# Kernel tuning notes

Hardware: AMD Instinct MI355X
Metric: run time of the kernel (lower is better)

The kernel has to match this reference:

```python
import jax, jax.numpy as jnp
import numpy as np

N = 6000; E = 96000; DIN = 3000; FH1 = 256; FH2 = 128; GH = 128; LAT = 256
K = 10; SCALE = 9; NC = 10; AT = 0.5; ALPHA = 1.0; BN_EPS = 1e-4

# eval-mode BatchNorm1d with running_mean=0, running_var=1
def _bn(x, g, b):
    return x * (g / jnp.sqrt(1.0 + BN_EPS)) + b

def _block(x, W, bb, g, be):  # Linear + BN(eval) + ELU (dropout=identity in eval)
    return jax.nn.elu(_bn(x @ W + bb, g, be))

def _tconv(x, src, dst, Wq, Wk, Wv, Ws, bq, bk, bv, bs):
    # PyG TransformerConv, heads=1, root_weight=True, eval (no dropout)
    q = x @ Wq + bq; k = x @ Wk + bk; v = x @ Wv + bv
    sc = 1.0 / jnp.sqrt(jnp.asarray(q.shape[-1], x.dtype))
    logit = jnp.sum(q[dst] * k[src], axis=-1) * sc            # [E]
    m = jax.ops.segment_max(logit, dst, num_segments=N)
    e = jnp.exp(logit - m[dst])
    s = jax.ops.segment_sum(e, dst, num_segments=N)
    alpha = e / s[dst]                                        # softmax over incoming edges
    out = jax.ops.segment_sum(alpha[:, None] * v[src], dst, num_segments=N) + x @ Ws + bs
    return out, alpha

def _dense_adj(src, dst, alpha):
    # remove_self_loops + to_dense_adj: dense[src, dst] += alpha for src != dst
    mask = (src != dst).astype(alpha.dtype)
    return jnp.zeros((N, N), alpha.dtype).at[src, dst].add(alpha * mask)

def _encode(x, adj, adjp, ew1, eb1, eg1, ebe1, ew2, eb2, eg2, ebe2,
            cWq, cWk, cWv, cWs, cbq, cbk, cbv, cbs):
    feat = _block(_block(x, ew1, eb1, eg1, ebe1), ew2, eb2, eg2, ebe2)
    h = feat
    lastAp = None
    for l in range(3):
        o, a = _tconv(h, adj[0], adj[1], cWq[l], cWk[l], cWv[l], cWs[l], cbq[l], cbk[l], cbv[l], cbs[l])
        # middle layer applies the 'prue' conv to the freshly produced x (as in source)
        hp_in = o if l == 1 else h
        op, ap = _tconv(hp_in, adjp[0], adjp[1], cWq[l], cWk[l], cWv[l], cWs[l], cbq[l], cbk[l], cbv[l], cbs[l])
        A = _dense_adj(adj[0], adj[1], a)
        Ap = _dense_adj(adjp[0], adjp[1], ap)
        h = (1.0 - AT) * (A @ o) + AT * (Ap @ op)
        if l < 2:
            h = jax.nn.relu(h)
        lastAp = Ap
    return h, feat, lastAp

def setup_inputs():
    key = jax.random.key(0)
    ks = jax.random.split(key, 24)
    w = lambda k, sh, fan: (jax.random.normal(k, sh, jnp.float32) / np.sqrt(fan)).astype(jnp.float32)
    inp = {}
    inp['x'] = jax.random.normal(ks[0], (N, DIN), jnp.float32)
    inp['x_neighbor'] = jax.random.normal(ks[1], (N, DIN), jnp.float32)
    inp['spatial'] = jax.random.uniform(ks[2], (N, 2), jnp.float32)
    inp['adj'] = jax.random.randint(ks[3], (2, E), 0, N, dtype=jnp.int32)
    inp['adj_prue'] = jax.random.randint(ks[4], (2, E), 0, N, dtype=jnp.int32)
    # encoder
    inp['enc_W1'] = w(ks[5], (DIN, FH1), DIN); inp['enc_b1'] = jnp.zeros((FH1,))
    inp['enc_g1'] = jnp.ones((FH1,)); inp['enc_be1'] = jnp.zeros((FH1,))
    inp['enc_W2'] = w(ks[6], (FH1, FH2), FH1); inp['enc_b2'] = jnp.zeros((FH2,))
    inp['enc_g2'] = jnp.ones((FH2,)); inp['enc_be2'] = jnp.zeros((FH2,))
    # 3 TransformerConv layers (gc1, conv_hidden[0], gc2) all 128->128: stacked
    inp['conv_Wq'] = w(ks[7], (3, GH, GH), GH); inp['conv_Wk'] = w(ks[8], (3, GH, GH), GH)
    inp['conv_Wv'] = w(ks[9], (3, GH, GH), GH); inp['conv_Ws'] = w(ks[10], (3, GH, GH), GH)
    inp['conv_bq'] = jnp.zeros((3, GH)); inp['conv_bk'] = jnp.zeros((3, GH))
    inp['conv_bv'] = jnp.zeros((3, GH)); inp['conv_bs'] = jnp.zeros((3, GH))
    # decoder
    inp['dec_W'] = w(ks[11], (LAT, DIN), LAT); inp['dec_b'] = jnp.zeros((DIN,))
    inp['dec_g'] = jnp.ones((DIN,)); inp['dec_be'] = jnp.zeros((DIN,))
    inp['cluster'] = w(ks[12], (NC, LAT), LAT)
    return inp

def reference(x, x_neighbor, spatial, enc_W1, enc_b1, enc_g1, enc_be1,
              enc_W2, enc_b2, enc_g2, enc_be2,
              conv_Wq, conv_Wk, conv_Wv, conv_Ws, conv_bq, conv_bk, conv_bv, conv_bs,
              dec_W, dec_b, dec_g, dec_be, cluster, adj, adj_prue):
    enc = (enc_W1, enc_b1, enc_g1, enc_be1, enc_W2, enc_b2, enc_g2, enc_be2)
    conv = (conv_Wq, conv_Wk, conv_Wv, conv_Ws, conv_bq, conv_bk, conv_bv, conv_bs)
    mu, feat_x, atten = _encode(x, adj, adj_prue, *enc, *conv)
    mu_nb, feat_nb, _ = _encode(x_neighbor, adj, adj_prue, *enc, *conv)
    z = jnp.concatenate([feat_x, mu], axis=1)          # [N, LAT]
    z_nb = jnp.concatenate([feat_nb, mu_nb], axis=1)
    # Graph_spatial: kNN in joint feature+spatial space (dense [N,N] distances)
    df = (jnp.sum(z * z, 1)[:, None] - 2.0 * (z @ z_nb.T) + jnp.sum(z_nb * z_nb, 1)[None, :])
    ds = (jnp.sum(spatial * spatial, 1)[:, None] - 2.0 * (spatial @ spatial.T)
          + jnp.sum(spatial * spatial, 1)[None, :])
    neg_top, idx_k = jax.lax.top_k(-(df + ds), K)      # [N, K]
    score_k = jax.nn.softmax(neg_top, axis=-1)
    # GCNBlock_spatial: gather scale=9 nearest neighbor features and aggregate
    idx9 = idx_k[:, :SCALE]
    x_h = z_nb[idx9]                                   # [N, 9, LAT]
    wgt = score_k[:, :SCALE]
    wgt = wgt / jnp.sum(wgt, axis=-1, keepdims=True)
    z_out = z + jnp.einsum('nk,nkd->nd', wgt, x_h)     # x1_lr
    x1_hr = (x_h * wgt[:, :, None]).reshape(N * SCALE, LAT)
    de_feat = _block(z_out, dec_W, dec_b, dec_g, dec_be)
    # student-t cluster assignment
    d2 = jnp.sum((z_out[:, None, :] - cluster[None, :, :]) ** 2, axis=2)
    q = (1.0 / (1.0 + d2 / ALPHA)) ** ((ALPHA + 1.0) / 2.0)
    q = q / jnp.sum(q, axis=1, keepdims=True)
    return (z_out, de_feat, q, feat_x, de_feat, x1_hr, atten)
```

## Files before the change

kernel.cpp:

```cpp
#include <hip/hip_runtime.h>
#include <hip/hip_bf16.h>
#include <math.h>
#include <stdint.h>

#define NN 6000
#define NE 96000
#define KDIN 3000
#define NCAND 12
#define NTILE 47
#define TCAND (NCAND*NTILE)
#define PRE 32

#define OFF_ZOUT 0
#define OFF_DE1  1536000
#define OFF_Q    19536000
#define OFF_FEAT 19596000
#define OFF_DE2  20364000
#define OFF_X1   38364000
#define OFF_ATT  52188000

typedef __attribute__((ext_vector_type(8))) short short8;
typedef __attribute__((ext_vector_type(4))) float f32x4;

__device__ __forceinline__ unsigned short f2bf(float f){
  unsigned int u = __float_as_uint(f);
  u += 0x7FFFu + ((u >> 16) & 1u);
  return (unsigned short)(u >> 16);
}
__device__ __forceinline__ float bf2f(unsigned short h){
  return __uint_as_float(((unsigned int)h) << 16);
}

__global__ void prep_k(const float* __restrict__ W1, const float* __restrict__ W2,
                       const float* __restrict__ Wq, const float* __restrict__ Wk,
                       const float* __restrict__ Wv, const float* __restrict__ Ws,
                       const float* __restrict__ bq, const float* __restrict__ bk,
                       const float* __restrict__ bv, const float* __restrict__ bs,
                       const float* __restrict__ decW, const float* __restrict__ spat,
                       double* __restrict__ W1t, double* __restrict__ W2t,
                       double* __restrict__ Bct, float* __restrict__ Dt,
                       double* __restrict__ bcat,
                       double* __restrict__ sx64, double* __restrict__ sy64,
                       double* __restrict__ ssq64,
                       float* __restrict__ sx32, float* __restrict__ sy32)
{
  int t = blockIdx.x * 256 + threadIdx.x;
  if (t < 768000){
    int n = t / 3000, k = t % 3000;
    W1t[t] = (double)W1[(size_t)k * 256 + n]; return;
  }
  t -= 768000;
  if (t < 32768){
    int n = t / 256, k = t % 256;
    W2t[t] = (double)W2[(size_t)k * 128 + n]; return;
  }
  t -= 32768;
  if (t < 196608){
    int l = t / 65536; int rem = t % 65536;
    int n = rem / 128, k = rem % 128;
    int sel = n >> 7, nn = n & 127;
    const float* Wm = sel==0 ? Wq : sel==1 ? Wk : sel==2 ? Wv : Ws;
    Bct[t] = (double)Wm[((size_t)(l*128) + k) * 128 + nn]; return;
  }
  t -= 196608;
  if (t < 768000){
    int n = t / 256, k = t % 256;
    Dt[t] = decW[(size_t)k * 3000 + n]; return;
  }
  t -= 768000;
  if (t < 1536){
    int l = t / 512, n = t % 512;
    int sel = n >> 7, nn = n & 127;
    const float* bm = sel==0 ? bq : sel==1 ? bk : sel==2 ? bv : bs;
    bcat[t] = (double)bm[l*128 + nn]; return;
  }
  t -= 1536;
  if (t < NN){
    float sx = spat[(size_t)t*2], sy = spat[(size_t)t*2+1];
    sx64[t]=(double)sx; sy64[t]=(double)sy;
    ssq64[t]=(double)sx*(double)sx + (double)sy*(double)sy;
    sx32[t]=sx; sy32[t]=sy; return;
  }
}

__global__ void castup_k(const float* __restrict__ s, double* __restrict__ d, int n){
  int t = blockIdx.x*256 + threadIdx.x;
  if (t < n) d[t] = (double)s[t];
}

__global__ void splitz_k(const double* __restrict__ z64, unsigned short* __restrict__ zh,
                         unsigned short* __restrict__ zl, int n){
  int t = blockIdx.x*256 + threadIdx.x;
  if (t < n){
    float v = (float)z64[t];
    unsigned short h = f2bf(v);
    float r = v - bf2f(h);
    zh[t] = h; zl[t] = f2bf(r);
  }
}

template<int EPI, typename TA>
__global__ __launch_bounds__(256)
void gemm64_k(const TA* __restrict__ A, int lda,
              const double* __restrict__ Bt, int ldb,
              int M, int K, int Ncol,
              double* __restrict__ outF, int ldc,
              const double* __restrict__ bias,
              const float* __restrict__ gam, const float* __restrict__ bet,
              double* __restrict__ outF2)
{
  __shared__ double lA[64][18];
  __shared__ double lB[64][18];
  const int tid = threadIdx.x;
  const int m0 = blockIdx.y * 64;
  const int n0 = blockIdx.x * 64;
  const int tx = tid & 15;
  const int ty = tid >> 4;

  double acc[4][4];
  #pragma unroll
  for (int i=0;i<4;i++)
    #pragma unroll
    for (int j=0;j<4;j++) acc[i][j] = 0.0;

  const int nkt = (K + 15) >> 4;
  for (int kt = 0; kt < nkt; kt++){
    const int k0 = kt << 4;
    __syncthreads();
    #pragma unroll
    for (int c=0;c<4;c++){
      int lin = tid + c*256;
      int row = lin >> 4, col = lin & 15;
      int gm = m0 + row, gk = k0 + col;
      double va = 0.0, vb = 0.0;
      if (gm < M && gk < K)        va = (double)A [(size_t)gm*lda + gk];
      if (n0+row < Ncol && gk < K) vb = Bt[(size_t)(n0+row)*ldb + gk];
      lA[row][col] = va;
      lB[row][col] = vb;
    }
    __syncthreads();
    #pragma unroll 4
    for (int kk=0; kk<16; kk+=2){
      double2 A0 = *(const double2*)&lA[ty   ][kk];
      double2 A1 = *(const double2*)&lA[ty+16][kk];
      double2 A2 = *(const double2*)&lA[ty+32][kk];
      double2 A3 = *(const double2*)&lA[ty+48][kk];
      double2 B0 = *(const double2*)&lB[tx   ][kk];
      double2 B1 = *(const double2*)&lB[tx+16][kk];
      double2 B2 = *(const double2*)&lB[tx+32][kk];
      double2 B3 = *(const double2*)&lB[tx+48][kk];
      acc[0][0]+=A0.x*B0.x; acc[0][1]+=A0.x*B1.x; acc[0][2]+=A0.x*B2.x; acc[0][3]+=A0.x*B3.x;
      acc[1][0]+=A1.x*B0.x; acc[1][1]+=A1.x*B1.x; acc[1][2]+=A1.x*B2.x; acc[1][3]+=A1.x*B3.x;
      acc[2][0]+=A2.x*B0.x; acc[2][1]+=A2.x*B1.x; acc[2][2]+=A2.x*B2.x; acc[2][3]+=A2.x*B3.x;
      acc[3][0]+=A3.x*B0.x; acc[3][1]+=A3.x*B1.x; acc[3][2]+=A3.x*B2.x; acc[3][3]+=A3.x*B3.x;
      acc[0][0]+=A0.y*B0.y; acc[0][1]+=A0.y*B1.y; acc[0][2]+=A0.y*B2.y; acc[0][3]+=A0.y*B3.y;
      acc[1][0]+=A1.y*B0.y; acc[1][1]+=A1.y*B1.y; acc[1][2]+=A1.y*B2.y; acc[1][3]+=A1.y*B3.y;
      acc[2][0]+=A2.y*B0.y; acc[2][1]+=A2.y*B1.y; acc[2][2]+=A2.y*B2.y; acc[2][3]+=A2.y*B3.y;
      acc[3][0]+=A3.y*B0.y; acc[3][1]+=A3.y*B1.y; acc[3][2]+=A3.y*B2.y; acc[3][3]+=A3.y*B3.y;
    }
  }
  #pragma unroll
  for (int j=0;j<4;j++){
    int gn = n0 + tx + 16*j;
    if (gn >= Ncol) continue;
    double bi = bias[gn];
    #pragma unroll
    for (int i=0;i<4;i++){
      int gm = m0 + ty + 16*i;
      if (gm >= M) continue;
      double v = acc[i][j] + bi;
      outF[(size_t)gm*ldc + gn] = v;
      if (outF2) outF2[(size_t)gm*ldc + gn] = v;
    }
  }
}

template<typename TA>
__global__ __launch_bounds__(256)
void gemm64s_k(const TA* __restrict__ A, int lda,
               const double* __restrict__ Bt, int ldb,
               int M, int K, int kchunk, int Ncol,
               double* __restrict__ part)
{
  __shared__ double lA[64][18];
  __shared__ double lB[64][18];
  const int tid = threadIdx.x;
  const int m0 = blockIdx.y * 64;
  const int n0 = blockIdx.x * 64;
  const int tx = tid & 15;
  const int ty = tid >> 4;
  const int kbeg = blockIdx.z * kchunk;
  const int kend = min(K, kbeg + kchunk);
  double* dst = part + (size_t)blockIdx.z * M * Ncol;

  double acc[4][4];
  #pragma unroll
  for (int i=0;i<4;i++)
    #pragma unroll
    for (int j=0;j<4;j++) acc[i][j] = 0.0;

  const int nkt = (kend - kbeg + 15) >> 4;
  for (int kt = 0; kt < nkt; kt++){
    const int k0 = kbeg + (kt << 4);
    __syncthreads();
    #pragma unroll
    for (int c=0;c<4;c++){
      int lin = tid + c*256;
      int row = lin >> 4, col = lin & 15;
      int gm = m0 + row, gk = k0 + col;
      double va = 0.0, vb = 0.0;
      if (gm < M && gk < kend)        va = (double)A [(size_t)gm*lda + gk];
      if (n0+row < Ncol && gk < kend) vb = Bt[(size_t)(n0+row)*ldb + gk];
      lA[row][col] = va;
      lB[row][col] = vb;
    }
    __syncthreads();
    #pragma unroll 4
    for (int kk=0; kk<16; kk+=2){
      double2 A0 = *(const double2*)&lA[ty   ][kk];
      double2 A1 = *(const double2*)&lA[ty+16][kk];
      double2 A2 = *(const double2*)&lA[ty+32][kk];
      double2 A3 = *(const double2*)&lA[ty+48][kk];
      double2 B0 = *(const double2*)&lB[tx   ][kk];
      double2 B1 = *(const double2*)&lB[tx+16][kk];
      double2 B2 = *(const double2*)&lB[tx+32][kk];
      double2 B3 = *(const double2*)&lB[tx+48][kk];
      acc[0][0]+=A0.x*B0.x; acc[0][1]+=A0.x*B1.x; acc[0][2]+=A0.x*B2.x; acc[0][3]+=A0.x*B3.x;
      acc[1][0]+=A1.x*B0.x; acc[1][1]+=A1.x*B1.x; acc[1][2]+=A1.x*B2.x; acc[1][3]+=A1.x*B3.x;
      acc[2][0]+=A2.x*B0.x; acc[2][1]+=A2.x*B1.x; acc[2][2]+=A2.x*B2.x; acc[2][3]+=A2.x*B3.x;
      acc[3][0]+=A3.x*B0.x; acc[3][1]+=A3.x*B1.x; acc[3][2]+=A3.x*B2.x; acc[3][3]+=A3.x*B3.x;
      acc[0][0]+=A0.y*B0.y; acc[0][1]+=A0.y*B1.y; acc[0][2]+=A0.y*B2.y; acc[0][3]+=A0.y*B3.y;
      acc[1][0]+=A1.y*B0.y; acc[1][1]+=A1.y*B1.y; acc[1][2]+=A1.y*B2.y; acc[1][3]+=A1.y*B3.y;
      acc[2][0]+=A2.y*B0.y; acc[2][1]+=A2.y*B1.y; acc[2][2]+=A2.y*B2.y; acc[2][3]+=A2.y*B3.y;
      acc[3][0]+=A3.y*B0.y; acc[3][1]+=A3.y*B1.y; acc[3][2]+=A3.y*B2.y; acc[3][3]+=A3.y*B3.y;
    }
  }
  #pragma unroll
  for (int j=0;j<4;j++){
    int gn = n0 + tx + 16*j;
    if (gn >= Ncol) continue;
    #pragma unroll
    for (int i=0;i<4;i++){
      int gm = m0 + ty + 16*i;
      if (gm >= M) continue;
      dst[(size_t)gm*Ncol + gn] = acc[i][j];
    }
  }
}

__global__ void epi64_k(const double* __restrict__ part, int nsplit, size_t pstride,
                        int M, int Ncol, const double* __restrict__ bias,
                        const float* __restrict__ gam, const float* __restrict__ bet,
                        double* __restrict__ out, int ldo)
{
  int t = blockIdx.x*256 + threadIdx.x;
  if (t >= M*Ncol) return;
  int gm = t / Ncol, gn = t - gm*Ncol;
  double v = 0.0;
  for (int s=0; s<nsplit; s++) v += part[(size_t)s*pstride + t];
  const double BNS = 0.99995000374968755261;
  v += bias[gn];
  v = v * ((double)gam[gn]*BNS) + (double)bet[gn];
  v = v > 0.0 ? v : expm1(v);
  out[(size_t)gm*ldo + gn] = v;
}

__global__ __launch_bounds__(256)
void gemm32d_k(const float* __restrict__ A, int lda,
               const float* __restrict__ Bt, int ldb,
               int M, int K, int Ncol,
               float* __restrict__ out1, int ldc,
               const float* __restrict__ bias, const float* __restrict__ gam,
               const float* __restrict__ bet, float* __restrict__ out2)
{
  __shared__ float lA[64][33];
  __shared__ float lB[64][33];
  const int tid = threadIdx.x;
  const int m0 = blockIdx.y * 64;
  const int n0 = blockIdx.x * 64;
  const int tx = tid & 15;
  const int ty = tid >> 4;

  float acc[4][4];
  #pragma unroll
  for (int i=0;i<4;i++)
    #pragma unroll
    for (int j=0;j<4;j++) acc[i][j] = 0.f;

  const int nkt = (K + 31) >> 5;
  for (int kt = 0; kt < nkt; kt++){
    const int k0 = kt << 5;
    __syncthreads();
    #pragma unroll
    for (int c=0;c<8;c++){
      int lin = tid + c*256;
      int row = lin >> 5, col = lin & 31;
      int gm = m0 + row, gk = k0 + col;
      float va = 0.f, vb = 0.f;
      if (gm < M && gk < K)        va = A [(size_t)gm*lda + gk];
      if (n0+row < Ncol && gk < K) vb = Bt[(size_t)(n0+row)*ldb + gk];
      lA[row][col] = va;
      lB[row][col] = vb;
    }
    __syncthreads();
    #pragma unroll 4
    for (int kk=0; kk<32; kk++){
      float a0=lA[ty][kk], a1=lA[ty+16][kk], a2=lA[ty+32][kk], a3=lA[ty+48][kk];
      float b0=lB[tx][kk], b1=lB[tx+16][kk], b2=lB[tx+32][kk], b3=lB[tx+48][kk];
      acc[0][0]+=a0*b0; acc[0][1]+=a0*b1; acc[0][2]+=a0*b2; acc[0][3]+=a0*b3;
      acc[1][0]+=a1*b0; acc[1][1]+=a1*b1; acc[1][2]+=a1*b2; acc[1][3]+=a1*b3;
      acc[2][0]+=a2*b0; acc[2][1]+=a2*b1; acc[2][2]+=a2*b2; acc[2][3]+=a2*b3;
      acc[3][0]+=a3*b0; acc[3][1]+=a3*b1; acc[3][2]+=a3*b2; acc[3][3]+=a3*b3;
    }
  }
  const float BNS = 0.99995000374968755f;
  #pragma unroll
  for (int j=0;j<4;j++){
    int gn = n0 + tx + 16*j;
    if (gn >= Ncol) continue;
    float bi = bias[gn];
    float gs = gam[gn]*BNS, be = bet[gn];
    #pragma unroll
    for (int i=0;i<4;i++){
      int gm = m0 + ty + 16*i;
      if (gm >= M) continue;
      float v = acc[i][j] + bi;
      v = v*gs + be; v = v > 0.f ? v : expm1f(v);
      out1[(size_t)gm*ldc + gn] = v;
      out2[(size_t)gm*ldc + gn] = v;
    }
  }
}

__global__ void csr_cnt_k(const int* __restrict__ key, int* __restrict__ cnt){
  int e = blockIdx.x*256 + threadIdx.x;
  if (e < NE) atomicAdd(&cnt[key[e]], 1);
}
__global__ __launch_bounds__(256)
void csr_scan_k(const int* __restrict__ cnt, int* __restrict__ rowptr, int* __restrict__ cursor){
  __shared__ int part[256];
  int t = threadIdx.x;
  int base = t*24;
  int loc[24]; int s=0;
  #pragma unroll
  for (int u=0;u<24;u++){
    int idx = base+u;
    int v = (idx<NN) ? cnt[idx] : 0;
    loc[u] = s; s += v;
  }
  part[t] = s;
  __syncthreads();
  if (t==0){
    int run=0;
    for (int u=0;u<256;u++){ int tmp=part[u]; part[u]=run; run+=tmp; }
  }
  __syncthreads();
  int off = part[t];
  #pragma unroll
  for (int u=0;u<24;u++){
    int idx = base+u;
    if (idx<NN){ rowptr[idx]=off+loc[u]; cursor[idx]=off+loc[u]; }
  }
  if (t==255) rowptr[NN] = off + s;
}
__global__ void csr_fill_k(const int* __restrict__ key, int* __restrict__ cursor,
                           int* __restrict__ elist){
  int e = blockIdx.x*256 + threadIdx.x;
  if (e < NE){ int pos = atomicAdd(&cursor[key[e]], 1); elist[pos] = e; }
}

__global__ __launch_bounds__(256)
void attn_k(double* __restrict__ QKVS, const int* __restrict__ rowptr,
            const int* __restrict__ elist, const int* __restrict__ src,
            double* __restrict__ alpha)
{
  __shared__ double lg[4][128];
  const int w = threadIdx.x >> 6;
  const int node = blockIdx.x*4 + w;
  if (node >= NN) return;
  const int lane = threadIdx.x & 63;
  const int e0 = rowptr[node], e1 = rowptr[node+1];
  const int deg = e1 - e0;
  if (deg <= 0) return;
  const double SC = 0.088388347648318447;
  const double* q = QKVS + (size_t)node*512;
  double q0 = q[lane], q1 = q[lane+64];

  if (deg <= 128){
    double m = -1.0e300;
    for (int i=0;i<deg;i++){
      const double* k = QKVS + (size_t)src[elist[e0+i]]*512 + 128;
      double p = q0*k[lane] + q1*k[lane+64];
      #pragma unroll
      for (int off=32; off; off>>=1) p += __shfl_xor(p, off);
      p *= SC;
      if (lane==0) lg[w][i] = p;
      m = fmax(m, p);
    }
    double S = 0.0;
    for (int i=0;i<deg;i++){
      double ex = exp(lg[w][i] - m);
      if (lane==0) lg[w][i] = ex;
      S += ex;
    }
    double inv = 1.0 / S;
    double o0 = QKVS[(size_t)node*512 + 384 + lane];
    double o1 = QKVS[(size_t)node*512 + 448 + lane];
    for (int i=0;i<deg;i++){
      int e = elist[e0+i];
      double a = lg[w][i] * inv;
      const double* v = QKVS + (size_t)src[e]*512 + 256;
      o0 = fma(a, v[lane],    o0);
      o1 = fma(a, v[lane+64], o1);
      if (lane==0) alpha[e] = a;
    }
    QKVS[(size_t)node*512 + 384 + lane] = o0;
    QKVS[(size_t)node*512 + 448 + lane] = o1;
  } else {
    double m = -1.0e300;
    for (int i=0;i<deg;i++){
      const double* k = QKVS + (size_t)src[elist[e0+i]]*512 + 128;
      double p = q0*k[lane] + q1*k[lane+64];
      #pragma unroll
      for (int off=32; off; off>>=1) p += __shfl_xor(p, off);
      m = fmax(m, p*SC);
    }
    double S = 0.0;
    for (int i=0;i<deg;i++){
      const double* k = QKVS + (size_t)src[elist[e0+i]]*512 + 128;
      double p = q0*k[lane] + q1*k[lane+64];
      #pragma unroll
      for (int off=32; off; off>>=1) p += __shfl_xor(p, off);
      S += exp(p*SC - m);
    }
    double inv = 1.0 / S;
    double o0 = QKVS[(size_t)node*512 + 384 + lane];
    double o1 = QKVS[(size_t)node*512 + 448 + lane];
    for (int i=0;i<deg;i++){
      int e = elist[e0+i];
      const double* k = QKVS + (size_t)src[e]*512 + 128;
      double p = q0*k[lane] + q1*k[lane+64];
      #pragma unroll
      for (int off=32; off; off>>=1) p += __shfl_xor(p, off);
      double a = exp(p*SC - m) * inv;
      const double* v = QKVS + (size_t)src[e]*512 + 256;
      o0 = fma(a, v[lane],    o0);
      o1 = fma(a, v[lane+64], o1);
      if (lane==0) alpha[e] = a;
    }
    QKVS[(size_t)node*512 + 384 + lane] = o0;
    QKVS[(size_t)node*512 + 448 + lane] = o1;
  }
}

__global__ __launch_bounds__(256)
void spmm_csr_k(const double* __restrict__ QK1, const double* __restrict__ QK2,
                const int* __restrict__ rpSA, const int* __restrict__ elSA,
                const int* __restrict__ dstA, const double* __restrict__ aA,
                const int* __restrict__ rpSP, const int* __restrict__ elSP,
                const int* __restrict__ dstP, const double* __restrict__ aP,
                double* __restrict__ out, int ldo, int offo, int dorelu)
{
  const int node = blockIdx.x*4 + (threadIdx.x>>6);
  if (node >= NN) return;
  const int lane = threadIdx.x & 63;
  double a0 = 0.0, a1 = 0.0;
  for (int idx = rpSA[node]; idx < rpSA[node+1]; ++idx){
    int e = elSA[idx]; int d = dstA[e];
    if (d != node){
      double wgt = 0.5 * aA[e];
      const double* o = QK1 + (size_t)d*512 + 384;
      a0 = fma(wgt, o[lane],    a0);
      a1 = fma(wgt, o[lane+64], a1);
    }
  }
  for (int idx = rpSP[node]; idx < rpSP[node+1]; ++idx){
    int e = elSP[idx]; int d = dstP[e];
    if (d != node){
      double wgt = 0.5 * aP[e];
      const double* o = QK2 + (size_t)d*512 + 384;
      a0 = fma(wgt, o[lane],    a0);
      a1 = fma(wgt, o[lane+64], a1);
    }
  }
  if (dorelu){ a0 = fmax(a0, 0.0); a1 = fmax(a1, 0.0); }
  out[(size_t)node*ldo + offo + lane]      = a0;
  out[(size_t)node*ldo + offo + 64 + lane] = a1;
}

__global__ void att_scatter_k(const int* __restrict__ src, const int* __restrict__ dst,
                              const double* __restrict__ alpha, float* __restrict__ att)
{
  int e = blockIdx.x*256 + threadIdx.x;
  if (e >= NE) return;
  int s = src[e], d = dst[e];
  if (s == d) return;
  atomicAdd(&att[(size_t)s*NN + d], (float)alpha[e]);
}

__global__ __launch_bounds__(256)
void distmf_k(const unsigned short* __restrict__ zXh, const unsigned short* __restrict__ zXl,
              const unsigned short* __restrict__ zNh, const unsigned short* __restrict__ zNl,
              const float* __restrict__ sxA, const float* __restrict__ syA,
              const float* __restrict__ cjA,
              float* __restrict__ candV, int* __restrict__ candI)
{
  __shared__ __align__(16) char smem[40960 + 1536];
  typedef unsigned short u16;
  u16 (*lAh)[40] = (u16(*)[40])(smem);
  u16 (*lAl)[40] = (u16(*)[40])(smem + 10240);
  u16 (*lBh)[40] = (u16(*)[40])(smem + 20480);
  u16 (*lBl)[40] = (u16(*)[40])(smem + 30720);
  float (*stile)[67] = (float(*)[67])(smem);
  float* sSx = (float*)(smem + 40960);
  float* sSy = sSx + 128;
  float* sC  = sSy + 128;

  const int tid = threadIdx.x;
  const int m0 = blockIdx.y * 128;
  const int n0 = blockIdx.x * 128;
  const int lane = tid & 63;
  const int wave = tid >> 6;
  const int wm = wave >> 1, wn = wave & 1;
  const int lr = lane & 15;
  const int lk = (lane >> 4) * 8;

  if (tid < 128){
    int jg = n0 + tid;
    if (jg < NN){ sSx[tid]=sxA[jg]; sSy[tid]=syA[jg]; sC[tid]=cjA[jg]; }
    else        { sSx[tid]=0.f; sSy[tid]=0.f; sC[tid]=-3e38f; }
  }

  f32x4 acc[4][4];
  #pragma unroll
  for (int i=0;i<4;i++)
    #pragma unroll
    for (int j=0;j<4;j++) acc[i][j] = (f32x4){0.f,0.f,0.f,0.f};

  for (int kt = 0; kt < 8; kt++){
    const int k0 = kt << 5;
    __syncthreads();
    #pragma unroll
    for (int c=0;c<4;c++){
      int lin = tid + c*256;
      int row = lin >> 3;
      int kc = (lin & 7) << 2;
      int gm = m0 + row, gn = n0 + row;
      ushort4 vh = {0,0,0,0}, vl = {0,0,0,0}, wh = {0,0,0,0}, wl = {0,0,0,0};
      if (gm < NN){
        vh = *(const ushort4*)(zXh + (size_t)gm*256 + k0 + kc);
        vl = *(const ushort4*)(zXl + (size_t)gm*256 + k0 + kc);
      }
      if (gn < NN){
        wh = *(const ushort4*)(zNh + (size_t)gn*256 + k0 + kc);
        wl = *(const ushort4*)(zNl + (size_t)gn*256 + k0 + kc);
      }
      *(ushort4*)&lAh[row][kc] = vh;
      *(ushort4*)&lAl[row][kc] = vl;
      *(ushort4*)&lBh[row][kc] = wh;
      *(ushort4*)&lBl[row][kc] = wl;
    }
    __syncthreads();
    short8 ah[4], al[4];
    #pragma unroll
    for (int fm=0; fm<4; fm++){
      ah[fm] = *(const short8*)&lAh[wm*64 + fm*16 + lr][lk];
      al[fm] = *(const short8*)&lAl[wm*64 + fm*16 + lr][lk];
    }
    #pragma unroll
    for (int fn=0; fn<4; fn++){
      short8 bh = *(const short8*)&lBh[wn*64 + fn*16 + lr][lk];
      short8 bl = *(const short8*)&lBl[wn*64 + fn*16 + lr][lk];
      #pragma unroll
      for (int fm=0; fm<4; fm++){
        acc[fm][fn] = __builtin_amdgcn_mfma_f32_16x16x32_bf16(ah[fm], bh, acc[fm][fn], 0,0,0);
        acc[fm][fn] = __builtin_amdgcn_mfma_f32_16x16x32_bf16(ah[fm], bl, acc[fm][fn], 0,0,0);
        acc[fm][fn] = __builtin_amdgcn_mfma_f32_16x16x32_bf16(al[fm], bh, acc[fm][fn], 0,0,0);
      }
    }
  }

  float tv[NCAND]; int ti[NCAND];
  #pragma unroll
  for (int p=0;p<NCAND;p++){ tv[p] = -3.4e38f; ti[p] = -1; }
  const int gi = m0 + tid;
  float sxi = 0.f, syi = 0.f;
  if (tid < 128 && gi < NN){ sxi = sxA[gi]; syi = syA[gi]; }

  for (int jh = 0; jh < 2; jh++){
    __syncthreads();
    if (wn == jh){
      #pragma unroll
      for (int fm=0;fm<4;fm++){
        #pragma unroll
        for (int fn=0;fn<4;fn++){
          int lrow = wm*64 + fm*16 + ((lane>>4)<<2);
          int lcol = fn*16 + lr;
          #pragma unroll
          for (int r=0;r<4;r++)
            stile[lrow + r][lcol] = acc[fm][fn][r];
        }
      }
    }
    __syncthreads();
    if (tid < 128 && gi < NN){
      #pragma unroll 1
      for (int jj=0; jj<64; jj++){
        int j = jh*64 + jj;
        float s = 2.f*stile[tid][jj] + 2.f*(sxi*sSx[j] + syi*sSy[j]) + sC[j];
        if (s > tv[NCAND-1]){
          bool g[NCAND];
          #pragma unroll
          for (int p=0;p<NCAND;p++) g[p] = s > tv[p];
          #pragma unroll
          for (int p=NCAND-1;p>0;--p) if (g[p-1]){ tv[p]=tv[p-1]; ti[p]=ti[p-1]; }
          #pragma unroll
          for (int p=0;p<NCAND;p++){ bool pl = g[p] && (p==0 || !g[p-1]); if (pl){ tv[p]=s; ti[p]=n0+j; } }
        }
      }
    }
  }
  if (tid < 128 && gi < NN){
    size_t base = ((size_t)gi*NTILE + blockIdx.x)*NCAND;
    #pragma unroll
    for (int p=0;p<NCAND;p++){ candV[base+p]=tv[p]; candI[base+p]=ti[p]; }
  }
}

__global__ __launch_bounds__(256)
void merge64_k(const float* __restrict__ candV, const int* __restrict__ candI,
               const double* __restrict__ Z, const double* __restrict__ Znb,
               const double* __restrict__ sx64, const double* __restrict__ sy64,
               double* __restrict__ wgt9, int* __restrict__ idx9)
{
  __shared__ double zi[256];
  __shared__ int    fjS[TCAND];
  __shared__ float  wbv[4];
  __shared__ int    wbc[4];
  __shared__ int    chosen;
  __shared__ int    pj[PRE];
  __shared__ double ps[PRE];

  const int i = blockIdx.x;
  const int t = threadIdx.x;
  const int lane = t & 63, wv = t >> 6;

  zi[t] = Z[(size_t)i*256 + t];

  float v0 = -3.4e38f, v1 = -3.4e38f, v2 = -3.4e38f;
  const int c0 = t, c1 = t + 256, c2 = t + 512;
  {
    float vv = candV[(size_t)i*TCAND + c0];
    int jj = candI[(size_t)i*TCAND + c0];
    fjS[c0] = jj;
    if (jj >= 0) v0 = vv;
  }
  if (c1 < TCAND){
    float vv = candV[(size_t)i*TCAND + c1];
    int jj = candI[(size_t)i*TCAND + c1];
    fjS[c1] = jj;
    if (jj >= 0) v1 = vv;
  }
  if (c2 < TCAND){
    float vv = candV[(size_t)i*TCAND + c2];
    int jj = candI[(size_t)i*TCAND + c2];
    fjS[c2] = jj;
    if (jj >= 0) v2 = vv;
  }
  __syncthreads();

  for (int it = 0; it < PRE; it++){
    float bv = v0; int bc = c0;
    if (v1 > bv || (v1 == bv && c1 < bc)){ bv = v1; bc = c1; }
    if (v2 > bv || (v2 == bv && c2 < bc)){ bv = v2; bc = c2; }
    #pragma unroll
    for (int off = 32; off; off >>= 1){
      float ov = __shfl_xor(bv, off);
      int   oc = __shfl_xor(bc, off);
      if (ov > bv || (ov == bv && oc < bc)){ bv = ov; bc = oc; }
    }
    if (lane == 0){ wbv[wv] = bv; wbc[wv] = bc; }
    __syncthreads();
    if (t == 0){
      float gb = wbv[0]; int gc = wbc[0];
      #pragma unroll
      for (int w2 = 1; w2 < 4; w2++)
        if (wbv[w2] > gb || (wbv[w2] == gb && wbc[w2] < gc)){ gb = wbv[w2]; gc = wbc[w2]; }
      chosen = gc;
      pj[it] = fjS[gc];
    }
    __syncthreads();
    int gc = chosen;
    if (c0 == gc) v0 = -3.4e38f;
    if (c1 == gc) v1 = -3.4e38f;
    if (c2 == gc) v2 = -3.4e38f;
  }

  const double sxi = sx64[i], syi = sy64[i];
  for (int c = wv; c < PRE; c += 4){
    int j = pj[c];
    const double* zj = Znb + (size_t)j*256;
    double p = 0.0;
    #pragma unroll
    for (int u = 0; u < 4; u++){
      double b = zj[lane + 64*u];
      double a = zi[lane + 64*u];
      p = fma(2.0*a - b, b, p);
    }
    #pragma unroll
    for (int off = 32; off; off >>= 1) p += __shfl_xor(p, off);
    double sxj = sx64[j], syj = sy64[j];
    double s = p + 2.0*(sxi*sxj + syi*syj) - (sxj*sxj + syj*syj);
    if (lane == 0) ps[c] = s;
  }
  __syncthreads();

  if (t == 0){
    double tv9[9]; int ti9[9];
    #pragma unroll
    for (int p = 0; p < 9; p++){ tv9[p] = -1.0e301; ti9[p] = 0x7FFFFFFF; }
    for (int c = 0; c < PRE; c++){
      double s = ps[c]; int j = pj[c];
      if (!((s > tv9[8]) || (s == tv9[8] && j < ti9[8]))) continue;
      int p = 8;
      while (p > 0 && ((s > tv9[p-1]) || (s == tv9[p-1] && j < ti9[p-1]))){
        tv9[p] = tv9[p-1]; ti9[p] = ti9[p-1]; --p;
      }
      tv9[p] = s; ti9[p] = j;
    }
    double m = tv9[0], e[9], S = 0.0;
    #pragma unroll
    for (int k = 0; k < 9; k++){ e[k] = exp(tv9[k] - m); S += e[k]; }
    #pragma unroll
    for (int k = 0; k < 9; k++){
      wgt9[(size_t)i*9 + k] = e[k] / S;
      idx9[(size_t)i*9 + k] = ti9[k];
    }
  }
}

__global__ __launch_bounds__(256)
void znbprep_k(const double* __restrict__ znb, const double* __restrict__ ssq64,
               float* __restrict__ cjA)
{
  __shared__ double red[256];
  int i = blockIdx.x, d = threadIdx.x;
  double v = znb[(size_t)i*256 + d];
  red[d] = v*v;
  __syncthreads();
  for (int s=128; s; s>>=1){ if (d<s) red[d]+=red[d+s]; __syncthreads(); }
  if (d==0) cjA[i] = -(float)(red[0] + ssq64[i]);
}
__global__ void featout_k(const double* __restrict__ z, float* __restrict__ o){
  int t = blockIdx.x*256+threadIdx.x;
  if (t < NN*128){ int i=t>>7, d=t&127; o[t] = (float)z[(size_t)i*256 + d]; }
}

__global__ __launch_bounds__(256)
void zout_k(const double* __restrict__ Z, const double* __restrict__ Znb,
            const int* __restrict__ idx9, const double* __restrict__ wgt9,
            float* __restrict__ zoOut, float* __restrict__ zoF32, float* __restrict__ x1)
{
  int i = blockIdx.x; int d = threadIdx.x;
  double a = Z[(size_t)i*256 + d];
  #pragma unroll
  for (int k=0;k<9;k++){
    int j = idx9[(size_t)i*9+k];
    double w = wgt9[(size_t)i*9+k];
    double t = w * Znb[(size_t)j*256 + d];
    a += t;
    x1[((size_t)i*9+k)*256 + d] = (float)t;
  }
  float af = (float)a;
  zoOut[(size_t)i*256+d] = af;
  zoF32[(size_t)i*256+d] = af;
}

__global__ __launch_bounds__(256)
void q_k(const float* __restrict__ zoF, const float* __restrict__ clus, float* __restrict__ qB)
{
  __shared__ float wred[10][4];
  __shared__ float qs[10];
  int i = blockIdx.x, d = threadIdx.x;
  int lane = d & 63, wv = d >> 6;
  float zo = zoF[(size_t)i*256 + d];
  #pragma unroll
  for (int c=0;c<10;c++){
    float df = zo - clus[(size_t)c*256 + d];
    float p = df*df;
    #pragma unroll
    for (int off=32; off; off>>=1) p += __shfl_down(p, off);
    if (lane == 0) wred[c][wv] = p;
  }
  __syncthreads();
  if (d < 10){
    float d2 = wred[d][0]+wred[d][1]+wred[d][2]+wred[d][3];
    qs[d] = 1.f/(1.f + d2);
  }
  __syncthreads();
  if (d < 10){
    float s = 0.f;
    #pragma unroll
    for (int c=0;c<10;c++) s += qs[c];
    qB[(size_t)i*10 + d] = qs[d]/s;
  }
}

extern "C" void kernel_launch(void* const* d_in, const int* in_sizes, int n_in,
                              void* d_out, int out_size, void* d_ws, size_t ws_size,
                              hipStream_t stream)
{
  (void)in_sizes; (void)n_in; (void)out_size; (void)ws_size;
  const float* x    = (const float*)d_in[0];
  const float* xnb  = (const float*)d_in[1];
  const float* spat = (const float*)d_in[2];
  const int*   adj  = (const int*)d_in[3];
  const int*   adjp = (const int*)d_in[4];
  const float* W1   = (const float*)d_in[5];
  const float* b1   = (const float*)d_in[6];
  const float* g1   = (const float*)d_in[7];
  const float* be1  = (const float*)d_in[8];
  const float* W2   = (const float*)d_in[9];
  const float* b2   = (const float*)d_in[10];
  const float* g2   = (const float*)d_in[11];
  const float* be2  = (const float*)d_in[12];
  const float* Wq   = (const float*)d_in[13];
  const float* Wk   = (const float*)d_in[14];
  const float* Wv   = (const float*)d_in[15];
  const float* Wsm  = (const float*)d_in[16];
  const float* bq   = (const float*)d_in[17];
  const float* bk   = (const float*)d_in[18];
  const float* bv   = (const float*)d_in[19];
  const float* bs   = (const float*)d_in[20];
  const float* decW = (const float*)d_in[21];
  const float* decb = (const float*)d_in[22];
  const float* decg = (const float*)d_in[23];
  const float* decbe= (const float*)d_in[24];
  const float* clus = (const float*)d_in[25];
  float* outF = (float*)d_out;
  const int* srcA = adj,  *dstA = adj + NE;
  const int* srcP = adjp, *dstP = adjp + NE;

  char* wsb = (char*)d_ws;
  size_t off = 0;
  auto alloc = [&](size_t bytes)->char*{
    char* p = wsb + off;
    off = (off + bytes + 255) & ~(size_t)255;
    return p;
  };
  double* W1t  = (double*)alloc(768000*8);
  double* W2t  = (double*)alloc(32768*8);
  double* Bct  = (double*)alloc(196608*8);
  float*  Dt   = (float*) alloc(768000*4);
  double* bcat = (double*)alloc(1536*8);
  double* sx64 = (double*)alloc(NN*8);
  double* sy64 = (double*)alloc(NN*8);
  double* ssq64= (double*)alloc(NN*8);
  float*  sx32 = (float*) alloc(NN*4);
  float*  sy32 = (float*) alloc(NN*4);
  double* b1c  = (double*)alloc(256*8);
  double* b2c  = (double*)alloc(128*8);
  double* H1   = (double*)alloc((size_t)NN*256*8);
  double* zX64 = (double*)alloc((size_t)NN*256*8);
  double* zNB64= (double*)alloc((size_t)NN*256*8);
  double* hcur = (double*)alloc((size_t)NN*128*8);
  double* QK1  = (double*)alloc((size_t)NN*512*8);
  double* QK2  = (double*)alloc((size_t)NN*512*8);
  double* alphaA=(double*)alloc((size_t)NE*8);
  double* alphaP=(double*)alloc((size_t)NE*8);
  double* part = (double*)alloc((size_t)4*NN*256*8);
  int* rpDA = (int*)alloc((NN+1)*4);
  int* rpDP = (int*)alloc((NN+1)*4);
  int* rpSA = (int*)alloc((NN+1)*4);
  int* rpSP = (int*)alloc((NN+1)*4);
  int* curDA= (int*)alloc(NN*4);
  int* curDP= (int*)alloc(NN*4);
  int* curSA= (int*)alloc(NN*4);
  int* curSP= (int*)alloc(NN*4);
  int* elDA = (int*)alloc(NE*4);
  int* elDP = (int*)alloc(NE*4);
  int* elSA = (int*)alloc(NE*4);
  int* elSP = (int*)alloc(NE*4);
  unsigned short* zXh = (unsigned short*)alloc((size_t)NN*256*2);
  unsigned short* zXl = (unsigned short*)alloc((size_t)NN*256*2);
  unsigned short* zNh = (unsigned short*)alloc((size_t)NN*256*2);
  unsigned short* zNl = (unsigned short*)alloc((size_t)NN*256*2);
  float*  cjA  = (float*) alloc(NN*4);
  float*  candV= (float*) alloc((size_t)NN*TCAND*4);
  int*    candI= (int*)   alloc((size_t)NN*TCAND*4);
  int*    idx9 = (int*)   alloc((size_t)NN*9*4);
  double* wgt9 = (double*)alloc((size_t)NN*9*8);
  float*  zoF32= (float*) alloc((size_t)NN*256*4);

  prep_k<<<6926, 256, 0, stream>>>(W1, W2, Wq, Wk, Wv, Wsm, bq, bk, bv, bs, decW, spat,
                                   W1t, W2t, Bct, Dt, bcat,
                                   sx64, sy64, ssq64, sx32, sy32);
  castup_k<<<1, 256, 0, stream>>>(b1, b1c, 256);
  castup_k<<<1, 256, 0, stream>>>(b2, b2c, 128);

  hipMemsetAsync(curDA, 0, NN*4, stream);
  hipMemsetAsync(curDP, 0, NN*4, stream);
  hipMemsetAsync(curSA, 0, NN*4, stream);
  hipMemsetAsync(curSP, 0, NN*4, stream);
  csr_cnt_k<<<375, 256, 0, stream>>>(dstA, curDA);
  csr_cnt_k<<<375, 256, 0, stream>>>(dstP, curDP);
  csr_cnt_k<<<375, 256, 0, stream>>>(srcA, curSA);
  csr_cnt_k<<<375, 256, 0, stream>>>(srcP, curSP);
  csr_scan_k<<<1, 256, 0, stream>>>(curDA, rpDA, curDA);
  csr_scan_k<<<1, 256, 0, stream>>>(curDP, rpDP, curDP);
  csr_scan_k<<<1, 256, 0, stream>>>(curSA, rpSA, curSA);
  csr_scan_k<<<1, 256, 0, stream>>>(curSP, rpSP, curSP);
  csr_fill_k<<<375, 256, 0, stream>>>(dstA, curDA, elDA);
  csr_fill_k<<<375, 256, 0, stream>>>(dstP, curDP, elDP);
  csr_fill_k<<<375, 256, 0, stream>>>(srcA, curSA, elSA);
  csr_fill_k<<<375, 256, 0, stream>>>(srcP, curSP, elSP);

  auto enc = [&](const float* xin, double* zbuf, bool isX){
    gemm64s_k<float><<<dim3(4,94,4), 256, 0, stream>>>(xin, KDIN, W1t, KDIN,
                                                       NN, KDIN, 768, 256, part);
    epi64_k<<<(NN*256+255)/256, 256, 0, stream>>>(part, 4, (size_t)NN*256,
                                                  NN, 256, b1c, g1, be1, H1, 256);
    gemm64s_k<double><<<dim3(2,94,4), 256, 0, stream>>>(H1, 256, W2t, 256,
                                                        NN, 256, 64, 128, part);
    epi64_k<<<(NN*128+255)/256, 256, 0, stream>>>(part, 4, (size_t)NN*128,
                                                  NN, 128, b2c, g2, be2, zbuf, 256);
    const double* hin = zbuf; int ldh = 256;
    for (int l=0; l<3; l++){
      const double* Bh = Bct + (size_t)l*65536;
      const double* bc = bcat + l*512;
      if (l != 1){
        gemm64_k<0,double><<<dim3(8,94), 256, 0, stream>>>(hin, ldh, Bh, 128, NN, 128, 512,
                                                           QK1, 512, bc, nullptr, nullptr, QK2);
        attn_k<<<1500, 256, 0, stream>>>(QK1, rpDA, elDA, srcA, alphaA);
        attn_k<<<1500, 256, 0, stream>>>(QK2, rpDP, elDP, srcP, alphaP);
      } else {
        gemm64_k<0,double><<<dim3(8,94), 256, 0, stream>>>(hin, ldh, Bh, 128, NN, 128, 512,
                                                           QK1, 512, bc, nullptr, nullptr, nullptr);
        attn_k<<<1500, 256, 0, stream>>>(QK1, rpDA, elDA, srcA, alphaA);
        gemm64_k<0,double><<<dim3(8,94), 256, 0, stream>>>(QK1 + 384, 512, Bh, 128, NN, 128, 512,
                                                           QK2, 512, bc, nullptr, nullptr, nullptr);
        attn_k<<<1500, 256, 0, stream>>>(QK2, rpDP, elDP, srcP, alphaP);
      }
      if (isX && l == 2){
        hipMemsetAsync(outF + (size_t)OFF_ATT, 0, (size_t)NN*NN*4, stream);
        att_scatter_k<<<375, 256, 0, stream>>>(srcP, dstP, alphaP, outF + (size_t)OFF_ATT);
      }
      if (l < 2){
        spmm_csr_k<<<1500, 256, 0, stream>>>(QK1, QK2, rpSA, elSA, dstA, alphaA,
                                             rpSP, elSP, dstP, alphaP, hcur, 128, 0, 1);
        hin = hcur; ldh = 128;
      } else {
        spmm_csr_k<<<1500, 256, 0, stream>>>(QK1, QK2, rpSA, elSA, dstA, alphaA,
                                             rpSP, elSP, dstP, alphaP, zbuf, 256, 128, 0);
      }
    }
  };
  enc(x,   zX64,  true);
  enc(xnb, zNB64, false);

  splitz_k<<<6000, 256, 0, stream>>>(zX64,  zXh, zXl, NN*256);
  splitz_k<<<6000, 256, 0, stream>>>(zNB64, zNh, zNl, NN*256);
  znbprep_k<<<NN, 256, 0, stream>>>(zNB64, ssq64, cjA);
  distmf_k<<<dim3(NTILE,47), 256, 0, stream>>>(zXh, zXl, zNh, zNl,
                                               sx32, sy32, cjA, candV, candI);
  merge64_k<<<NN, 256, 0, stream>>>(candV, candI, zX64, zNB64, sx64, sy64, wgt9, idx9);

  zout_k<<<NN, 256, 0, stream>>>(zX64, zNB64, idx9, wgt9,
                                 outF + (size_t)OFF_ZOUT, zoF32, outF + (size_t)OFF_X1);
  gemm32d_k<<<dim3(47,94), 256, 0, stream>>>(zoF32, 256, Dt, 256, NN, 256, 3000,
                                             outF + (size_t)OFF_DE1, 3000, decb, decg, decbe,
                                             outF + (size_t)OFF_DE2);
  q_k<<<NN, 256, 0, stream>>>(zoF32, clus, outF + (size_t)OFF_Q);
  featout_k<<<3000, 256, 0, stream>>>(zX64, outF + (size_t)OFF_FEAT);
}
```

Measured before the change: 2.861 ms.

## Batch both encoder passes into single launches over stacked node sets

The two encoder invocations (x and xnb) are merged so every GEMM, attention and SpMM kernel processes 2*NN rows in one launch. The first GEMM reads from two input pointers, and the attention and SpMM kernels offset node indices and alpha arrays for the second graph copy. This halves the number of launches and doubles the grid size for kernels that previously underfilled the GPU, at the cost of doubled scratch buffers.

```diff
diff --git a/kernel.cpp b/kernel.cpp
--- a/kernel.cpp
+++ b/kernel.cpp
@@ -177,7 +177,7 @@
 
 template<typename TA>
 __global__ __launch_bounds__(256)
-void gemm64s_k(const TA* __restrict__ A, int lda,
+void gemm64s_k(const TA* __restrict__ A, const TA* __restrict__ A2, int M1, int lda,
                const double* __restrict__ Bt, int ldb,
                int M, int K, int kchunk, int Ncol,
                double* __restrict__ part)
@@ -209,7 +209,10 @@
       int row = lin >> 4, col = lin & 15;
       int gm = m0 + row, gk = k0 + col;
       double va = 0.0, vb = 0.0;
-      if (gm < M && gk < kend)        va = (double)A [(size_t)gm*lda + gk];
+      if (gm < M && gk < kend){
+        va = (gm < M1) ? (double)A[(size_t)gm*lda + gk]
+                       : (double)A2[(size_t)(gm-M1)*lda + gk];
+      }
       if (n0+row < Ncol && gk < kend) vb = Bt[(size_t)(n0+row)*ldb + gk];
       lA[row][col] = va;
       lB[row][col] = vb;
@@ -219,7 +222,7 @@
     for (int kk=0; kk<16; kk+=2){
       double2 A0 = *(const double2*)&lA[ty   ][kk];
       double2 A1 = *(const double2*)&lA[ty+16][kk];
-      double2 A2 = *(const double2*)&lA[ty+32][kk];
+      double2 A2v = *(const double2*)&lA[ty+32][kk];
       double2 A3 = *(const double2*)&lA[ty+48][kk];
       double2 B0 = *(const double2*)&lB[tx   ][kk];
       double2 B1 = *(const double2*)&lB[tx+16][kk];
@@ -227,11 +230,11 @@
       double2 B3 = *(const double2*)&lB[tx+48][kk];
       acc[0][0]+=A0.x*B0.x; acc[0][1]+=A0.x*B1.x; acc[0][2]+=A0.x*B2.x; acc[0][3]+=A0.x*B3.x;
       acc[1][0]+=A1.x*B0.x; acc[1][1]+=A1.x*B1.x; acc[1][2]+=A1.x*B2.x; acc[1][3]+=A1.x*B3.x;
-      acc[2][0]+=A2.x*B0.x; acc[2][1]+=A2.x*B1.x; acc[2][2]+=A2.x*B2.x; acc[2][3]+=A2.x*B3.x;
+      acc[2][0]+=A2v.x*B0.x; acc[2][1]+=A2v.x*B1.x; acc[2][2]+=A2v.x*B2.x; acc[2][3]+=A2v.x*B3.x;
       acc[3][0]+=A3.x*B0.x; acc[3][1]+=A3.x*B1.x; acc[3][2]+=A3.x*B2.x; acc[3][3]+=A3.x*B3.x;
       acc[0][0]+=A0.y*B0.y; acc[0][1]+=A0.y*B1.y; acc[0][2]+=A0.y*B2.y; acc[0][3]+=A0.y*B3.y;
       acc[1][0]+=A1.y*B0.y; acc[1][1]+=A1.y*B1.y; acc[1][2]+=A1.y*B2.y; acc[1][3]+=A1.y*B3.y;
-      acc[2][0]+=A2.y*B0.y; acc[2][1]+=A2.y*B1.y; acc[2][2]+=A2.y*B2.y; acc[2][3]+=A2.y*B3.y;
+      acc[2][0]+=A2v.y*B0.y; acc[2][1]+=A2v.y*B1.y; acc[2][2]+=A2v.y*B2.y; acc[2][3]+=A2v.y*B3.y;
       acc[3][0]+=A3.y*B0.y; acc[3][1]+=A3.y*B1.y; acc[3][2]+=A3.y*B2.y; acc[3][3]+=A3.y*B3.y;
     }
   }
@@ -377,9 +380,12 @@
   __shared__ double lg[4][128];
   const int w = threadIdx.x >> 6;
   const int node = blockIdx.x*4 + w;
-  if (node >= NN) return;
+  if (node >= 2*NN) return;
+  const int base = (node < NN) ? 0 : NN;
+  const int aoff = (node < NN) ? 0 : NE;
+  const int cn = node - base;
   const int lane = threadIdx.x & 63;
-  const int e0 = rowptr[node], e1 = rowptr[node+1];
+  const int e0 = rowptr[cn], e1 = rowptr[cn+1];
   const int deg = e1 - e0;
   if (deg <= 0) return;
   const double SC = 0.088388347648318447;
@@ -389,7 +395,7 @@
   if (deg <= 128){
     double m = -1.0e300;
     for (int i=0;i<deg;i++){
-      const double* k = QKVS + (size_t)src[elist[e0+i]]*512 + 128;
+      const double* k = QKVS + (size_t)(src[elist[e0+i]] + base)*512 + 128;
       double p = q0*k[lane] + q1*k[lane+64];
       #pragma unroll
       for (int off=32; off; off>>=1) p += __shfl_xor(p, off);
@@ -409,17 +415,17 @@
     for (int i=0;i<deg;i++){
       int e = elist[e0+i];
       double a = lg[w][i] * inv;
-      const double* v = QKVS + (size_t)src[e]*512 + 256;
+      const double* v = QKVS + (size_t)(src[e] + base)*512 + 256;
       o0 = fma(a, v[lane],    o0);
       o1 = fma(a, v[lane+64], o1);
-      if (lane==0) alpha[e] = a;
+      if (lane==0) alpha[aoff + e] = a;
     }
     QKVS[(size_t)node*512 + 384 + lane] = o0;
     QKVS[(size_t)node*512 + 448 + lane] = o1;
   } else {
     double m = -1.0e300;
     for (int i=0;i<deg;i++){
-      const double* k = QKVS + (size_t)src[elist[e0+i]]*512 + 128;
+      const double* k = QKVS + (size_t)(src[elist[e0+i]] + base)*512 + 128;
       double p = q0*k[lane] + q1*k[lane+64];
       #pragma unroll
       for (int off=32; off; off>>=1) p += __shfl_xor(p, off);
@@ -427,7 +433,7 @@
     }
     double S = 0.0;
     for (int i=0;i<deg;i++){
-      const double* k = QKVS + (size_t)src[elist[e0+i]]*512 + 128;
+      const double* k = QKVS + (size_t)(src[elist[e0+i]] + base)*512 + 128;
       double p = q0*k[lane] + q1*k[lane+64];
       #pragma unroll
       for (int off=32; off; off>>=1) p += __shfl_xor(p, off);
@@ -438,15 +444,15 @@
     double o1 = QKVS[(size_t)node*512 + 448 + lane];
     for (int i=0;i<deg;i++){
       int e = elist[e0+i];
-      const double* k = QKVS + (size_t)src[e]*512 + 128;
+      const double* k = QKVS + (size_t)(src[e] + base)*512 + 128;
       double p = q0*k[lane] + q1*k[lane+64];
       #pragma unroll
       for (int off=32; off; off>>=1) p += __shfl_xor(p, off);
       double a = exp(p*SC - m) * inv;
-      const double* v = QKVS + (size_t)src[e]*512 + 256;
+      const double* v = QKVS + (size_t)(src[e] + base)*512 + 256;
       o0 = fma(a, v[lane],    o0);
       o1 = fma(a, v[lane+64], o1);
-      if (lane==0) alpha[e] = a;
+      if (lane==0) alpha[aoff + e] = a;
     }
     QKVS[(size_t)node*512 + 384 + lane] = o0;
     QKVS[(size_t)node*512 + 448 + lane] = o1;
@@ -462,23 +468,26 @@
                 double* __restrict__ out, int ldo, int offo, int dorelu)
 {
   const int node = blockIdx.x*4 + (threadIdx.x>>6);
-  if (node >= NN) return;
+  if (node >= 2*NN) return;
+  const int base = (node < NN) ? 0 : NN;
+  const int aoff = (node < NN) ? 0 : NE;
+  const int cn = node - base;
   const int lane = threadIdx.x & 63;
   double a0 = 0.0, a1 = 0.0;
-  for (int idx = rpSA[node]; idx < rpSA[node+1]; ++idx){
+  for (int idx = rpSA[cn]; idx < rpSA[cn+1]; ++idx){
     int e = elSA[idx]; int d = dstA[e];
-    if (d != node){
-      double wgt = 0.5 * aA[e];
-      const double* o = QK1 + (size_t)d*512 + 384;
+    if (d != cn){
+      double wgt = 0.5 * aA[aoff + e];
+      const double* o = QK1 + (size_t)(d + base)*512 + 384;
       a0 = fma(wgt, o[lane],    a0);
       a1 = fma(wgt, o[lane+64], a1);
     }
   }
-  for (int idx = rpSP[node]; idx < rpSP[node+1]; ++idx){
+  for (int idx = rpSP[cn]; idx < rpSP[cn+1]; ++idx){
     int e = elSP[idx]; int d = dstP[e];
-    if (d != node){
-      double wgt = 0.5 * aP[e];
-      const double* o = QK2 + (size_t)d*512 + 384;
+    if (d != cn){
+      double wgt = 0.5 * aP[aoff + e];
+      const double* o = QK2 + (size_t)(d + base)*512 + 384;
       a0 = fma(wgt, o[lane],    a0);
       a1 = fma(wgt, o[lane+64], a1);
     }
@@ -860,15 +869,14 @@
   float*  sy32 = (float*) alloc(NN*4);
   double* b1c  = (double*)alloc(256*8);
   double* b2c  = (double*)alloc(128*8);
-  double* H1   = (double*)alloc((size_t)NN*256*8);
-  double* zX64 = (double*)alloc((size_t)NN*256*8);
-  double* zNB64= (double*)alloc((size_t)NN*256*8);
-  double* hcur = (double*)alloc((size_t)NN*128*8);
-  double* QK1  = (double*)alloc((size_t)NN*512*8);
-  double* QK2  = (double*)alloc((size_t)NN*512*8);
-  double* alphaA=(double*)alloc((size_t)NE*8);
-  double* alphaP=(double*)alloc((size_t)NE*8);
-  double* part = (double*)alloc((size_t)4*NN*256*8);
+  double* H1   = (double*)alloc((size_t)2*NN*256*8);
+  double* zAll = (double*)alloc((size_t)2*NN*256*8);
+  double* hcur = (double*)alloc((size_t)2*NN*128*8);
+  double* QK1  = (double*)alloc((size_t)2*NN*512*8);
+  double* QK2  = (double*)alloc((size_t)2*NN*512*8);
+  double* alphaA=(double*)alloc((size_t)2*NE*8);
+  double* alphaP=(double*)alloc((size_t)2*NE*8);
+  double* part = (double*)alloc((size_t)4*2*NN*256*8);
   int* rpDA = (int*)alloc((NN+1)*4);
   int* rpDP = (int*)alloc((NN+1)*4);
   int* rpSA = (int*)alloc((NN+1)*4);
@@ -892,6 +900,9 @@
   double* wgt9 = (double*)alloc((size_t)NN*9*8);
   float*  zoF32= (float*) alloc((size_t)NN*256*4);
 
+  double* zX64  = zAll;
+  double* zNB64 = zAll + (size_t)NN*256;
+
   prep_k<<<6926, 256, 0, stream>>>(W1, W2, Wq, Wk, Wv, Wsm, bq, bk, bv, bs, decW, spat,
                                    W1t, W2t, Bct, Dt, bcat,
                                    sx64, sy64, ssq64, sx32, sy32);
@@ -915,48 +926,47 @@
   csr_fill_k<<<375, 256, 0, stream>>>(srcA, curSA, elSA);
   csr_fill_k<<<375, 256, 0, stream>>>(srcP, curSP, elSP);
 
-  auto enc = [&](const float* xin, double* zbuf, bool isX){
-    gemm64s_k<float><<<dim3(4,94,4), 256, 0, stream>>>(xin, KDIN, W1t, KDIN,
-                                                       NN, KDIN, 768, 256, part);
-    epi64_k<<<(NN*256+255)/256, 256, 0, stream>>>(part, 4, (size_t)NN*256,
-                                                  NN, 256, b1c, g1, be1, H1, 256);
-    gemm64s_k<double><<<dim3(2,94,4), 256, 0, stream>>>(H1, 256, W2t, 256,
-                                                        NN, 256, 64, 128, part);
-    epi64_k<<<(NN*128+255)/256, 256, 0, stream>>>(part, 4, (size_t)NN*128,
-                                                  NN, 128, b2c, g2, be2, zbuf, 256);
-    const double* hin = zbuf; int ldh = 256;
-    for (int l=0; l<3; l++){
-      const double* Bh = Bct + (size_t)l*65536;
-      const double* bc = bcat + l*512;
-      if (l != 1){
-        gemm64_k<0,double><<<dim3(8,94), 256, 0, stream>>>(hin, ldh, Bh, 128, NN, 128, 512,
-                                                           QK1, 512, bc, nullptr, nullptr, QK2);
-        attn_k<<<1500, 256, 0, stream>>>(QK1, rpDA, elDA, srcA, alphaA);
-        attn_k<<<1500, 256, 0, stream>>>(QK2, rpDP, elDP, srcP, alphaP);
-      } else {
-        gemm64_k<0,double><<<dim3(8,94), 256, 0, stream>>>(hin, ldh, Bh, 128, NN, 128, 512,
-                                                           QK1, 512, bc, nullptr, nullptr, nullptr);
-        attn_k<<<1500, 256, 0, stream>>>(QK1, rpDA, elDA, srcA, alphaA);
-        gemm64_k<0,double><<<dim3(8,94), 256, 0, stream>>>(QK1 + 384, 512, Bh, 128, NN, 128, 512,
-                                                           QK2, 512, bc, nullptr, nullptr, nullptr);
-        attn_k<<<1500, 256, 0, stream>>>(QK2, rpDP, elDP, srcP, alphaP);
-      }
-      if (isX && l == 2){
-        hipMemsetAsync(outF + (size_t)OFF_ATT, 0, (size_t)NN*NN*4, stream);
-        att_scatter_k<<<375, 256, 0, stream>>>(srcP, dstP, alphaP, outF + (size_t)OFF_ATT);
-      }
-      if (l < 2){
-        spmm_csr_k<<<1500, 256, 0, stream>>>(QK1, QK2, rpSA, elSA, dstA, alphaA,
-                                             rpSP, elSP, dstP, alphaP, hcur, 128, 0, 1);
-        hin = hcur; ldh = 128;
-      } else {
-        spmm_csr_k<<<1500, 256, 0, stream>>>(QK1, QK2, rpSA, elSA, dstA, alphaA,
-                                             rpSP, elSP, dstP, alphaP, zbuf, 256, 128, 0);
-      }
-    }
-  };
-  enc(x,   zX64,  true);
-  enc(xnb, zNB64, false);
+  const int M2 = 2*NN;
+
+  gemm64s_k<float><<<dim3(4,188,4), 256, 0, stream>>>(x, xnb, NN, KDIN, W1t, KDIN,
+                                                      M2, KDIN, 768, 256, part);
+  epi64_k<<<(M2*256+255)/256, 256, 0, stream>>>(part, 4, (size_t)M2*256,
+                                                M2, 256, b1c, g1, be1, H1, 256);
+  gemm64s_k<double><<<dim3(2,188,4), 256, 0, stream>>>(H1, H1, M2, 256, W2t, 256,
+                                                       M2, 256, 64, 128, part);
+  epi64_k<<<(M2*128+255)/256, 256, 0, stream>>>(part, 4, (size_t)M2*128,
+                                                M2, 128, b2c, g2, be2, zAll, 256);
+
+  const double* hin = zAll; int ldh = 256;
+  for (int l=0; l<3; l++){
+    const double* Bh = Bct + (size_t)l*65536;
+    const double* bc = bcat + l*512;
+    if (l != 1){
+      gemm64_k<0,double><<<dim3(8,188), 256, 0, stream>>>(hin, ldh, Bh, 128, M2, 128, 512,
+                                                          QK1, 512, bc, nullptr, nullptr, QK2);
+      attn_k<<<3000, 256, 0, stream>>>(QK1, rpDA, elDA, srcA, alphaA);
+      attn_k<<<3000, 256, 0, stream>>>(QK2, rpDP, elDP, srcP, alphaP);
+    } else {
+      gemm64_k<0,double><<<dim3(8,188), 256, 0, stream>>>(hin, ldh, Bh, 128, M2, 128, 512,
+                                                          QK1, 512, bc, nullptr, nullptr, nullptr);
+      attn_k<<<3000, 256, 0, stream>>>(QK1, rpDA, elDA, srcA, alphaA);
+      gemm64_k<0,double><<<dim3(8,188), 256, 0, stream>>>(QK1 + 384, 512, Bh, 128, M2, 128, 512,
+                                                          QK2, 512, bc, nullptr, nullptr, nullptr);
+      attn_k<<<3000, 256, 0, stream>>>(QK2, rpDP, elDP, srcP, alphaP);
+    }
+    if (l == 2){
+      hipMemsetAsync(outF + (size_t)OFF_ATT, 0, (size_t)NN*NN*4, stream);
+      att_scatter_k<<<375, 256, 0, stream>>>(srcP, dstP, alphaP, outF + (size_t)OFF_ATT);
+    }
+    if (l < 2){
+      spmm_csr_k<<<3000, 256, 0, stream>>>(QK1, QK2, rpSA, elSA, dstA, alphaA,
+                                           rpSP, elSP, dstP, alphaP, hcur, 128, 0, 1);
+      hin = hcur; ldh = 128;
+    } else {
+      spmm_csr_k<<<3000, 256, 0, stream>>>(QK1, QK2, rpSA, elSA, dstA, alphaA,
+                                           rpSP, elSP, dstP, alphaP, zAll, 256, 128, 0);
+    }
+  }
 
   splitz_k<<<6000, 256, 0, stream>>>(zX64,  zXh, zXl, NN*256);
   splitz_k<<<6000, 256, 0, stream>>>(zNB64, zNh, zNl, NN*256);
```

Result: faster. 2.658 ms (-7.1%).
